# Performance work log

Hardware: AMD Instinct MI355X
Metric: run time of the kernel (lower is better)

Reference implementation:

```python
import jax, jax.numpy as jnp
import numpy as np

KERNEL = (7, 7)
NUM_CH = 4
EPS = 1e-06
ROPE_BASE = 10000.0


def _rel_dist():
    coords = [np.arange(k, dtype=np.float32) - k // 2 for k in KERNEL]
    g = np.meshgrid(*coords, indexing='ij')
    d = np.sqrt(sum(gi ** 2 for gi in g))
    return jnp.asarray(d.reshape(-1)), float(d.max())


def silu(x):
    return x * jax.nn.sigmoid(x)


def rmsnorm(x, w):
    rms = jnp.sqrt(jnp.mean(x * x, axis=-1, keepdims=True) + EPS)
    return x / rms * w


def apply_rope(x):
    # x: (B, L, H, D); positions run over dim -2 (matches torch default)
    H, D = x.shape[-2], x.shape[-1]
    half = D // 2
    pos = jnp.arange(H, dtype=jnp.float32)
    freqs = 1.0 / (ROPE_BASE ** (jnp.arange(half, dtype=x.dtype) / half))
    ang = pos[:, None] * freqs  # (H, half)
    cos, sin = jnp.cos(ang), jnp.sin(ang)
    x1, x2 = x[..., :half], x[..., half:2 * half]
    return jnp.concatenate([x1 * cos - x2 * sin, x1 * sin + x2 * cos], axis=-1)


def unfold2d(x):
    # x: (B, Hs, Ws, C) -> (B, Hs, Ws, k1*k2, C), row-major kernel order
    B, Hs, Ws, C = x.shape
    k1, k2 = KERNEL
    xp = jnp.pad(x, ((0, 0), ((k1 - 1) // 2, k1 // 2), ((k2 - 1) // 2, k2 // 2), (0, 0)))
    wins = [xp[:, i:i + Hs, j:j + Ws, :] for i in range(k1) for j in range(k2)]
    return jnp.stack(wins, axis=3)


def setup_inputs() -> dict:
    key = jax.random.key(0)
    ks = jax.random.split(key, 8)
    C = 256
    x = jax.random.normal(ks[0], (2, 64, 64, C), dtype=jnp.float32)
    W_qkv = jax.random.normal(ks[1], (C, 3 * C), dtype=jnp.float32) * 0.02
    w_qnorm = jnp.ones((C // NUM_CH,), dtype=jnp.float32)
    w_knorm = jnp.ones((C // NUM_CH,), dtype=jnp.float32)
    W_wp = jax.random.normal(ks[2], (C, 2 * NUM_CH), dtype=jnp.float32) * 0.02
    b_wp = jax.random.normal(ks[3], (2 * NUM_CH,), dtype=jnp.float32) * 0.02
    w_onorm = jnp.ones((C,), dtype=jnp.float32)
    W_out = jax.random.normal(ks[4], (C, C), dtype=jnp.float32) * 0.02
    W_gate = jax.random.normal(ks[5], (C, C), dtype=jnp.float32) * 0.02
    b_gate = 2.0 * jnp.ones((C,), dtype=jnp.float32)
    return {"x": x, "W_qkv": W_qkv, "w_qnorm": w_qnorm, "w_knorm": w_knorm,
            "W_wp": W_wp, "b_wp": b_wp, "w_onorm": w_onorm, "W_out": W_out,
            "W_gate": W_gate, "b_gate": b_gate}


def reference(x, W_qkv, w_qnorm, w_knorm, W_wp, b_wp, w_onorm, W_out, W_gate, b_gate):
    rel_dist, max_dist = _rel_dist()
    B, Hs, Ws, C = x.shape
    L = Hs * Ws
    H = NUM_CH
    D = C // H
    Wsz = KERNEL[0] * KERNEL[1]
    scale = D ** (-0.5)

    qkv = silu(x @ W_qkv)
    q, k, v = jnp.split(qkv, 3, axis=-1)

    q_flat = apply_rope(rmsnorm(q.reshape(B, L, H, D), w_qnorm))
    k_flat = apply_rope(rmsnorm(k.reshape(B, L, H, D), w_knorm))
    k = k_flat.reshape(B, Hs, Ws, C)

    wp = silu(x @ W_wp + b_wp)  # (B, Hs, Ws, 2H)
    width_raw, sharp_raw = jnp.split(wp, 2, axis=-1)
    width = jax.nn.sigmoid(width_raw) * max_dist + 0.5
    sharpness = jax.nn.sigmoid(sharp_raw) * 9.5 + 0.5

    k_win = unfold2d(k).reshape(B, L, Wsz, H, D)
    v_win = unfold2d(v).reshape(B, L, Wsz, H, D)

    scores = jnp.einsum('blhd,blwhd->blhw', q_flat, k_win) * scale
    width_f = width.reshape(B, L, H, 1)
    sharp_f = sharpness.reshape(B, L, H, 1)
    soft_mask = jax.nn.sigmoid((width_f - rel_dist) * sharp_f)
    scores = scores - (1.0 - soft_mask) * 10000.0
    attn = jax.nn.softmax(scores, axis=-1)

    out = jnp.einsum('blhw,blwhd->blhd', attn, v_win).reshape(B, Hs, Ws, C)
    out = rmsnorm(out, w_onorm)

    gate = jax.nn.sigmoid(silu(v @ W_gate + b_gate))
    merged = gate * v + (1.0 - gate) * out
    return silu(merged @ W_out)
```

## Files before the change

### kernel.cpp

```cpp
#include <hip/hip_runtime.h>
#include <hip/hip_fp16.h>
#include <math.h>

__device__ __forceinline__ float sigm(float x)  { return 1.0f / (1.0f + __expf(-x)); }
__device__ __forceinline__ float siluf(float x) { return x * sigm(x); }

typedef _Float16 half8  __attribute__((ext_vector_type(8)));
typedef _Float16 half4  __attribute__((ext_vector_type(4)));
typedef float    f32x4  __attribute__((ext_vector_type(4)));

__device__ __forceinline__ void gld16(const void* g, void* l) {
    __builtin_amdgcn_global_load_lds(
        (const __attribute__((address_space(1))) unsigned*)g,
        (__attribute__((address_space(3))) unsigned*)l, 16, 0, 0);
}

template <int MI, int AMODE>
__device__ __forceinline__ void gemm_core16(
    const __half* __restrict__ A16,
    const __half* __restrict__ Bhi, const __half* __restrict__ Blo,
    int nbs, int m0, int n0, int t, f32x4 (&acc)[MI][4])
{
    __shared__ short As[MI * 1024], BsHi[4096], BsLo[4096];
    const int lane = t & 63, wave = t >> 6;
    const int wm = (wave >> 1) * (MI << 4), wn = (wave & 1) << 6;
    const int fr = lane & 15, fq = lane >> 4;

    for (int kb = 0; kb < 8; ++kb) {
        __syncthreads();
#pragma unroll
        for (int hf = 0; hf < MI / 2; ++hf) {
            const int rr = wave * (MI << 3) + (hf << 4);
            size_t ga;
            if (AMODE == 0)
                ga = (((size_t)(kb * 8192 + m0 + rr)) << 5) + (lane << 3);
            else
                ga = (((size_t)(m0 + rr + (lane >> 2))) << 8) + (kb << 5) + ((lane & 3) << 3);
            gld16(A16 + ga, &As[rr << 5]);
        }
#pragma unroll
        for (int hf = 0; hf < 2; ++hf) {
            const int rr = (wave << 5) + (hf << 4);
            const size_t gb = (((size_t)(kb * nbs + n0 + rr)) << 5) + (lane << 3);
            gld16(Bhi + gb, &BsHi[rr << 5]);
            gld16(Blo + gb, &BsLo[rr << 5]);
        }
        __syncthreads();

        half8 a[MI], bh[4], bl[4];
#pragma unroll
        for (int i = 0; i < MI; ++i)
            a[i] = *(const half8*)&As[((wm + (i << 4) + fr) << 5) + (fq << 3)];
#pragma unroll
        for (int i = 0; i < 4; ++i) {
            const int boff = ((wn + (i << 4) + fr) << 5) + (fq << 3);
            bh[i] = *(const half8*)&BsHi[boff];
            bl[i] = *(const half8*)&BsLo[boff];
        }
#pragma unroll
        for (int mi = 0; mi < MI; ++mi)
#pragma unroll
            for (int ni = 0; ni < 4; ++ni) {
                acc[mi][ni] = __builtin_amdgcn_mfma_f32_16x16x32_f16(a[mi], bh[ni], acc[mi][ni], 0, 0, 0);
                acc[mi][ni] = __builtin_amdgcn_mfma_f32_16x16x32_f16(a[mi], bl[ni], acc[mi][ni], 0, 0, 0);
            }
    }
}

__global__ __launch_bounds__(256) void prep_kernel(
    const float* __restrict__ x, const float* __restrict__ Wqkv,
    const float* __restrict__ Wgate, const float* __restrict__ Wout,
    const float* __restrict__ Wwp, const float* __restrict__ bwp,
    __half* __restrict__ xh,
    __half* __restrict__ wqh, __half* __restrict__ wql,
    __half* __restrict__ wgh, __half* __restrict__ wgl,
    __half* __restrict__ woh, __half* __restrict__ wol,
    float* __restrict__ width, float* __restrict__ sharp)
{
    __shared__ float xs[32][260];
    const int t = threadIdx.x;
    const int blk = blockIdx.x;
    if (blk < 256) {
        const int row0 = blk << 5;
        for (int e = t; e < 2048; e += 256) {
            int r = e >> 6, cc = (e & 63) << 2;
            *(float4*)&xs[r][cc] = *(const float4*)&x[(size_t)(row0 + r) * 256 + cc];
        }
        __syncthreads();
        const int r = t >> 3, kb = t & 7;
        __half hibuf[32];
#pragma unroll
        for (int i = 0; i < 32; ++i)
            hibuf[i] = __float2half(xs[r][(kb << 5) + i]);
        const size_t ob = ((size_t)(kb * 8192 + row0 + r)) << 5;
#pragma unroll
        for (int i = 0; i < 4; ++i)
            *(int4*)&xh[ob + (i << 3)] = *(int4*)&hibuf[i << 3];
        float acc = 0.f;
#pragma unroll 8
        for (int k = 0; k < 256; ++k) acc += xs[r][k] * Wwp[k * 8 + kb];
        float s = sigm(siluf(acc + bwp[kb]));
        const int row = row0 + r;
        if (kb < 4) width[row * 4 + kb] = s * 4.242640687119285f + 0.5f;
        else        sharp[row * 4 + kb - 4] = s * 9.5f + 0.5f;
    } else {
        const float* W; __half *Whi, *Wlo; int N, nb0, ncnt;
        if (blk < 288)      { W = Wqkv;  Whi = wqh; Wlo = wql; N = 768; nb0 = (blk - 256) * 24; ncnt = 24; }
        else if (blk < 296) { W = Wgate; Whi = wgh; Wlo = wgl; N = 256; nb0 = (blk - 288) * 32; ncnt = 32; }
        else                { W = Wout;  Whi = woh; Wlo = wol; N = 256; nb0 = (blk - 296) * 32; ncnt = 32; }
        for (int j = 0; j < ncnt; ++j)
            xs[j][t] = W[(size_t)t * N + nb0 + j];
        __syncthreads();
        for (int c = t; c < ncnt * 8; c += 256) {
            const int j = c >> 3, kb = c & 7;
            __half hibuf[32], lobuf[32];
#pragma unroll
            for (int i = 0; i < 32; ++i) {
                float v = xs[j][(kb << 5) + i];
                __half hv = __float2half(v);
                hibuf[i] = hv;
                lobuf[i] = __float2half(v - __half2float(hv));
            }
            const size_t ob = ((size_t)(kb * N + nb0 + j)) << 5;
#pragma unroll
            for (int i = 0; i < 4; ++i) {
                *(int4*)&Whi[ob + (i << 3)] = *(int4*)&hibuf[i << 3];
                *(int4*)&Wlo[ob + (i << 3)] = *(int4*)&lobuf[i << 3];
            }
        }
    }
}

__global__ __launch_bounds__(256, 3) void gemm_qkv(
    const __half* __restrict__ xh,
    const __half* __restrict__ wqh, const __half* __restrict__ wql,
    const float* __restrict__ wq, const float* __restrict__ wk,
    __half* __restrict__ qh, __half* __restrict__ kh, __half* __restrict__ vh)
{
    const int t  = threadIdx.x;
    const int m0 = blockIdx.y << 7, n0 = blockIdx.x << 7;
    f32x4 acc[4][4] = {};
    gemm_core16<4, 0>(xh, wqh, wql, 768, m0, n0, t, acc);

    const int lane = t & 63, wave = t >> 6;
    const int wm = (wave >> 1) << 6, wn = (wave & 1) << 6;
    const int fr = lane & 15, fq = lane >> 4;
    const int gc0 = n0 + wn;
    const int seg = gc0 >> 8;
    const int h   = (gc0 >> 6) & 3;
    const int hc0 = h << 6;

#pragma unroll
    for (int mi = 0; mi < 4; ++mi)
#pragma unroll
        for (int ni = 0; ni < 4; ++ni)
#pragma unroll
            for (int r = 0; r < 4; ++r)
                acc[mi][ni][r] = siluf(acc[mi][ni][r]);

    if (seg == 2) {
#pragma unroll
        for (int mi = 0; mi < 4; ++mi)
#pragma unroll
            for (int r = 0; r < 4; ++r) {
                const size_t row = m0 + wm + (mi << 4) + (fq << 2) + r;
#pragma unroll
                for (int ni = 0; ni < 4; ++ni)
                    vh[row * 256 + hc0 + (ni << 4) + fr] = __float2half(acc[mi][ni][r]);
            }
    } else {
        const float* wnorm = seg ? wk : wq;
        float wv[4];
#pragma unroll
        for (int ni = 0; ni < 4; ++ni) wv[ni] = wnorm[(ni << 4) + fr];
        float cs[2], sn[2];
#pragma unroll
        for (int j = 0; j < 2; ++j) {
            const int d = (j << 4) + fr;
            const float freq = powf(10000.f, -(float)d * (1.f / 32.f));
            const float ang = (float)h * freq;
            cs[j] = cosf(ang); sn[j] = sinf(ang);
        }
        __half* dstbase = (seg ? kh : qh);
#pragma unroll
        for (int mi = 0; mi < 4; ++mi)
#pragma unroll
            for (int r = 0; r < 4; ++r) {
                float ss = acc[mi][0][r] * acc[mi][0][r] + acc[mi][1][r] * acc[mi][1][r]
                         + acc[mi][2][r] * acc[mi][2][r] + acc[mi][3][r] * acc[mi][3][r];
                ss += __shfl_xor(ss, 1); ss += __shfl_xor(ss, 2);
                ss += __shfl_xor(ss, 4); ss += __shfl_xor(ss, 8);
                const float rinv = 1.f / sqrtf(ss * (1.f / 64.f) + 1e-6f);
                float xv[4];
#pragma unroll
                for (int ni = 0; ni < 4; ++ni) xv[ni] = acc[mi][ni][r] * rinv * wv[ni];
                const float o0 = xv[0] * cs[0] - xv[2] * sn[0];
                const float o2 = xv[0] * sn[0] + xv[2] * cs[0];
                const float o1 = xv[1] * cs[1] - xv[3] * sn[1];
                const float o3 = xv[1] * sn[1] + xv[3] * cs[1];
                const size_t row = m0 + wm + (mi << 4) + (fq << 2) + r;
                __half* dst = dstbase + row * 256 + hc0;
                dst[fr]      = __float2half(o0);
                dst[16 + fr] = __float2half(o1);
                dst[32 + fr] = __float2half(o2);
                dst[48 + fr] = __float2half(o3);
            }
    }
}

__global__ __launch_bounds__(256, 3) void gemm_gate(
    const __half* __restrict__ vh,
    const __half* __restrict__ wgh, const __half* __restrict__ wgl,
    const float* __restrict__ bias, const float* __restrict__ attn_o,
    const float* __restrict__ sumsq4, const float* __restrict__ w_onorm,
    __half* __restrict__ mh)
{
    const int t  = threadIdx.x;
    const int m0 = blockIdx.y << 6, n0 = blockIdx.x << 7;
    f32x4 acc[2][4] = {};
    gemm_core16<2, 1>(vh, wgh, wgl, 256, m0, n0, t, acc);

    const int lane = t & 63, wave = t >> 6;
    const int wm = (wave >> 1) << 5, wn = (wave & 1) << 6;
    const int fr = lane & 15, fq = lane >> 4;

    float rmsf[2][4];
#pragma unroll
    for (int mi = 0; mi < 2; ++mi)
#pragma unroll
        for (int r = 0; r < 4; ++r) {
            const int m = m0 + wm + (mi << 4) + (fq << 2) + r;
            float4 s4 = *(const float4*)&sumsq4[(size_t)m * 4];
            rmsf[mi][r] = 1.f / sqrtf((s4.x + s4.y + s4.z + s4.w) * (1.f / 256.f) + 1e-6f);
        }

#pragma unroll
    for (int mi = 0; mi < 2; ++mi)
#pragma unroll
        for (int ni = 0; ni < 4; ++ni) {
            const int n  = n0 + wn + (ni << 4) + fr;
            const int mb = m0 + wm + (mi << 4) + (fq << 2);
            const float bb  = bias[n];
            const float won = w_onorm[n];
#pragma unroll
            for (int r = 0; r < 4; ++r) {
                const int m = mb + r;
                const float g  = sigm(siluf(acc[mi][ni][r] + bb));
                const float vv = __half2float(vh[(size_t)m * 256 + n]);
                const float oo = attn_o[(size_t)m * 256 + n] * rmsf[mi][r] * won;
                mh[(size_t)m * 256 + n] = __float2half(g * vv + (1.f - g) * oo);
            }
        }
}

__global__ __launch_bounds__(256, 3) void gemm_out(
    const __half* __restrict__ mh,
    const __half* __restrict__ woh, const __half* __restrict__ wol,
    float* __restrict__ out)
{
    const int t  = threadIdx.x;
    const int m0 = blockIdx.y << 6, n0 = blockIdx.x << 7;
    f32x4 acc[2][4] = {};
    gemm_core16<2, 1>(mh, woh, wol, 256, m0, n0, t, acc);

    const int lane = t & 63, wave = t >> 6;
    const int wm = (wave >> 1) << 5, wn = (wave & 1) << 6;
    const int fr = lane & 15, fq = lane >> 4;
#pragma unroll
    for (int mi = 0; mi < 2; ++mi)
#pragma unroll
        for (int ni = 0; ni < 4; ++ni) {
            const int n  = n0 + wn + (ni << 4) + fr;
            const int mb = m0 + wm + (mi << 4) + (fq << 2);
#pragma unroll
            for (int r = 0; r < 4; ++r)
                out[(size_t)(mb + r) * 256 + n] = siluf(acc[mi][ni][r]);
        }
}

#define PT 208

__global__ __launch_bounds__(256, 3) void attn_mfma(
    const __half* __restrict__ qh, const __half* __restrict__ kh,
    const __half* __restrict__ vh, const float* __restrict__ width,
    const float* __restrict__ sharp, float* __restrict__ attn_o,
    float* __restrict__ sumsq4)
{
    __shared__ short smem[26624];
    short* Ksh = smem;
    short* Psh = smem;
    short* Vt  = smem + 13312;

    const int t = threadIdx.x;
    const int lane = t & 63, wave = t >> 6;
    const int fr = lane & 15, fq = lane >> 4;
    const int patch = blockIdx.x, h = blockIdx.y, b = blockIdx.z;
    const int pr0 = (patch >> 3) << 3, pc0 = (patch & 7) << 3;
    const size_t cbase = (((size_t)b << 20)) + ((size_t)h << 6);

    float wd[4], sh[4]; int lq[4];
#pragma unroll
    for (int r = 0; r < 4; ++r) {
        const int q = (wave << 4) + (fq << 2) + r;
        lq[r] = (pr0 + (q >> 3)) * 64 + pc0 + (q & 7);
        wd[r] = width[((b << 12) + lq[r]) * 4 + h];
        sh[r] = sharp[((b << 12) + lq[r]) * 4 + h];
    }

    {
        const int lr = lane >> 3;
        const int doff = (((lane & 7) ^ (lr & 7)) << 3);
#pragma unroll
        for (int ci = 0; ci < 7; ++ci) {
            const int c = wave + (ci << 2);
            if (c < 26) {
                const int pr = (c << 3) + lr;
                const int pi = pr / 14, pj = pr - pi * 14;
                const int grc = min(max(pr0 - 3 + pi, 0), 63);
                const int gcc = min(max(pc0 - 3 + pj, 0), 63);
                gld16(kh + cbase + (size_t)((grc << 6) + gcc) * 256 + doff,
                      &Ksh[c << 9]);
            }
        }
    }

    const int qrow = (wave << 4) + fr;
    const int lqr = (pr0 + (qrow >> 3)) * 64 + pc0 + (qrow & 7);
    const __half* qptr = qh + (((size_t)(b << 12) + lqr) << 8) + (h << 6) + (fq << 3);
    half8 a0 = *(const half8*)qptr;
    half8 a1 = *(const half8*)(qptr + 32);

    const int srow = t >> 5;
    const int d2 = (t & 31) << 1;
    unsigned v0[13], v1[13];
#pragma unroll
    for (int j = 0; j < 13; ++j) {
        const int p = (j << 4) + (srow << 1);
#pragma unroll
        for (int e = 0; e < 2; ++e) {
            const int pp = p + e;
            const int pi = pp / 14, pj = pp - pi * 14;
            const int gr = pr0 - 3 + pi, gc = pc0 - 3 + pj;
            const bool ok = (pp < 196) & ((unsigned)gr < 64u) & ((unsigned)gc < 64u);
            const int grc = min(max(gr, 0), 63), gcc = min(max(gc, 0), 63);
            const unsigned vv = *(const unsigned*)(vh + cbase + (size_t)((grc << 6) + gcc) * 256 + d2);
            (e ? v1 : v0)[j] = ok ? vv : 0u;
        }
    }
#pragma unroll
    for (int j = 0; j < 13; ++j) {
        const int p = (j << 4) + (srow << 1);
        const unsigned lo = (v0[j] & 0xffffu) | (v1[j] << 16);
        const unsigned hi = (v0[j] >> 16) | (v1[j] & 0xffff0000u);
        *(unsigned*)&Vt[d2 * PT + p]       = lo;
        *(unsigned*)&Vt[(d2 + 1) * PT + p] = hi;
    }
    __syncthreads();

    f32x4 sc[13];
#pragma unroll
    for (int tl = 0; tl < 13; ++tl) {
        const int kr = (tl << 4) + fr;
        half8 b0 = *(const half8*)&Ksh[(kr << 6) + (((0 + fq) ^ (kr & 7)) << 3)];
        half8 b1 = *(const half8*)&Ksh[(kr << 6) + (((4 + fq) ^ (kr & 7)) << 3)];
        f32x4 z = {0.f, 0.f, 0.f, 0.f};
        z = __builtin_amdgcn_mfma_f32_16x16x32_f16(a0, b0, z, 0, 0, 0);
        sc[tl] = __builtin_amdgcn_mfma_f32_16x16x32_f16(a1, b1, z, 0, 0, 0);
    }

    float mx[4] = {-3e38f, -3e38f, -3e38f, -3e38f};
#pragma unroll
    for (int tl = 0; tl < 13; ++tl) {
        const int p = (tl << 4) + fr;
        const int pi = p / 14, pj = p - pi * 14;
        const bool pvld = p < 196;
        const bool inb = pvld & ((unsigned)(pr0 - 3 + pi) < 64u) & ((unsigned)(pc0 - 3 + pj) < 64u);
#pragma unroll
        for (int r = 0; r < 4; ++r) {
            const int q = (wave << 4) + (fq << 2) + r;
            const int di = pi - 3 - ((q >> 3) & 7), dj = pj - 3 - (q & 7);
            const bool win = pvld & ((unsigned)(di + 3) <= 6u) & ((unsigned)(dj + 3) <= 6u);
            const float rel = sqrtf((float)(di * di + dj * dj));
            const float mk = sigm((wd[r] - rel) * sh[r]);
            const float s0 = inb ? sc[tl][r] * 0.125f : 0.f;
            float s = s0 - (1.f - mk) * 10000.f;
            s = win ? s : -3e38f;
            sc[tl][r] = s;
            mx[r] = fmaxf(mx[r], s);
        }
    }
#pragma unroll
    for (int r = 0; r < 4; ++r) {
        mx[r] = fmaxf(mx[r], __shfl_xor(mx[r], 1));
        mx[r] = fmaxf(mx[r], __shfl_xor(mx[r], 2));
        mx[r] = fmaxf(mx[r], __shfl_xor(mx[r], 4));
        mx[r] = fmaxf(mx[r], __shfl_xor(mx[r], 8));
    }
    float sm[4] = {0.f, 0.f, 0.f, 0.f};
#pragma unroll
    for (int tl = 0; tl < 13; ++tl)
#pragma unroll
        for (int r = 0; r < 4; ++r) {
            const float e = __expf(sc[tl][r] - mx[r]);
            sc[tl][r] = e; sm[r] += e;
        }
#pragma unroll
    for (int r = 0; r < 4; ++r) {
        sm[r] += __shfl_xor(sm[r], 1);
        sm[r] += __shfl_xor(sm[r], 2);
        sm[r] += __shfl_xor(sm[r], 4);
        sm[r] += __shfl_xor(sm[r], 8);
        sm[r] = 1.f / sm[r];
    }

    __syncthreads();
#pragma unroll
    for (int tl = 0; tl < 13; ++tl)
#pragma unroll
        for (int r = 0; r < 4; ++r) {
            __half pv = __float2half(sc[tl][r] * sm[r]);
            Psh[((wave << 4) + (fq << 2) + r) * PT + (tl << 4) + fr] = *(short*)&pv;
        }
    asm volatile("s_waitcnt lgkmcnt(0)" ::: "memory");

    f32x4 o[4] = {};
    const int pra = (wave << 4) + fr;
#pragma unroll
    for (int s = 0; s < 6; ++s) {
        half8 pa = *(const half8*)&Psh[pra * PT + (fq << 3) + (s << 5)];
#pragma unroll
        for (int dt = 0; dt < 4; ++dt) {
            half8 vbf = *(const half8*)&Vt[((dt << 4) + fr) * PT + (fq << 3) + (s << 5)];
            o[dt] = __builtin_amdgcn_mfma_f32_16x16x32_f16(pa, vbf, o[dt], 0, 0, 0);
        }
    }
    {
        half4 pa = *(const half4*)&Psh[pra * PT + 192 + (fq << 2)];
#pragma unroll
        for (int dt = 0; dt < 4; ++dt) {
            half4 vbf = *(const half4*)&Vt[((dt << 4) + fr) * PT + 192 + (fq << 2)];
            o[dt] = __builtin_amdgcn_mfma_f32_16x16x16f16(pa, vbf, o[dt], 0, 0, 0);
        }
    }

#pragma unroll
    for (int r = 0; r < 4; ++r) {
        float ss = o[0][r]*o[0][r] + o[1][r]*o[1][r] + o[2][r]*o[2][r] + o[3][r]*o[3][r];
        ss += __shfl_xor(ss, 1); ss += __shfl_xor(ss, 2);
        ss += __shfl_xor(ss, 4); ss += __shfl_xor(ss, 8);
        const size_t rowb = (((size_t)(b << 12) + lq[r]) << 8) + h * 64;
#pragma unroll
        for (int dt = 0; dt < 4; ++dt)
            attn_o[rowb + (dt << 4) + fr] = o[dt][r];
        if (fr == 0) sumsq4[(((b << 12) + lq[r]) << 2) + h] = ss;
    }
}

extern "C" void kernel_launch(void* const* d_in, const int* in_sizes, int n_in,
                              void* d_out, int out_size, void* d_ws, size_t ws_size,
                              hipStream_t stream)
{
    const float* x      = (const float*)d_in[0];
    const float* W_qkv  = (const float*)d_in[1];
    const float* w_qn   = (const float*)d_in[2];
    const float* w_kn   = (const float*)d_in[3];
    const float* W_wp   = (const float*)d_in[4];
    const float* b_wp   = (const float*)d_in[5];
    const float* w_on   = (const float*)d_in[6];
    const float* W_out  = (const float*)d_in[7];
    const float* W_gate = (const float*)d_in[8];
    const float* b_gate = (const float*)d_in[9];
    float* out = (float*)d_out;

    __half* ws16 = (__half*)d_ws;
    __half* xh  = ws16;
    __half* wqh = xh  + 2097152;
    __half* wql = wqh + 196608;
    __half* wgh = wql + 196608;
    __half* wgl = wgh + 65536;
    __half* woh = wgl + 65536;
    __half* wol = woh + 65536;
    __half* qhp = wol + 65536;
    __half* khp = qhp + 2097152;
    __half* vhp = khp + 2097152;
    __half* mh  = vhp + 2097152;
    float* attn_o = (float*)(mh + 2097152);
    float* widthp = attn_o + 2097152;
    float* sharpp = widthp + 32768;
    float* sumsq4 = sharpp + 32768;

    prep_kernel<<<304, 256, 0, stream>>>(x, W_qkv, W_gate, W_out, W_wp, b_wp,
                                         xh, wqh, wql, wgh, wgl, woh, wol,
                                         widthp, sharpp);
    gemm_qkv<<<dim3(6, 64), 256, 0, stream>>>(xh, wqh, wql, w_qn, w_kn,
                                              qhp, khp, vhp);
    attn_mfma<<<dim3(64, 4, 2), 256, 0, stream>>>(qhp, khp, vhp, widthp, sharpp,
                                                  attn_o, sumsq4);
    gemm_gate<<<dim3(2, 128), 256, 0, stream>>>(vhp, wgh, wgl, b_gate,
                                                attn_o, sumsq4, w_on, mh);
    gemm_out<<<dim3(2, 128), 256, 0, stream>>>(mh, woh, wol, out);
}
```

Baseline: 156.6 us.

## Load K directly into registers and split P staging to cut LDS use

The attention kernel no longer stages the K window in shared memory. Each lane now loads its K fragments straight from global memory into registers, in three batches interleaved with the QK MFMAs. The probability tile is written to LDS in two halves of seven and six column tiles, each followed by a partial PV product, so the P buffer shrinks. Together these cut LDS from about 52KB to 40KB and raise the occupancy hint from 3 to 4 blocks. In exchange there is more register pressure, possible spills under the tighter launch bound, uncoalesced repeated K reads from global memory, and an extra barrier.

```diff
diff --git a/kernel.cpp b/kernel.cpp
--- a/kernel.cpp
+++ b/kernel.cpp
@@ -278,25 +278,25 @@
         }
 }
 
-#define PT 208
-
-__global__ __launch_bounds__(256, 3) void attn_mfma(
+#define PTV 208
+#define PTP 112
+
+__global__ __launch_bounds__(256, 4) void attn_mfma(
     const __half* __restrict__ qh, const __half* __restrict__ kh,
     const __half* __restrict__ vh, const float* __restrict__ width,
     const float* __restrict__ sharp, float* __restrict__ attn_o,
     float* __restrict__ sumsq4)
 {
-    __shared__ short smem[26624];
-    short* Ksh = smem;
-    short* Psh = smem;
-    short* Vt  = smem + 13312;
+    __shared__ short smem[20480];
+    short* Vt  = smem;
+    short* Psh = smem + 13312;
 
     const int t = threadIdx.x;
     const int lane = t & 63, wave = t >> 6;
     const int fr = lane & 15, fq = lane >> 4;
     const int patch = blockIdx.x, h = blockIdx.y, b = blockIdx.z;
     const int pr0 = (patch >> 3) << 3, pc0 = (patch & 7) << 3;
-    const size_t cbase = (((size_t)b << 20)) + ((size_t)h << 6);
+    const size_t cb0 = ((size_t)b << 20) + ((size_t)h << 6);
 
     float wd[4], sh[4]; int lq[4];
 #pragma unroll
@@ -306,29 +306,6 @@
         wd[r] = width[((b << 12) + lq[r]) * 4 + h];
         sh[r] = sharp[((b << 12) + lq[r]) * 4 + h];
     }
-
-    {
-        const int lr = lane >> 3;
-        const int doff = (((lane & 7) ^ (lr & 7)) << 3);
-#pragma unroll
-        for (int ci = 0; ci < 7; ++ci) {
-            const int c = wave + (ci << 2);
-            if (c < 26) {
-                const int pr = (c << 3) + lr;
-                const int pi = pr / 14, pj = pr - pi * 14;
-                const int grc = min(max(pr0 - 3 + pi, 0), 63);
-                const int gcc = min(max(pc0 - 3 + pj, 0), 63);
-                gld16(kh + cbase + (size_t)((grc << 6) + gcc) * 256 + doff,
-                      &Ksh[c << 9]);
-            }
-        }
-    }
-
-    const int qrow = (wave << 4) + fr;
-    const int lqr = (pr0 + (qrow >> 3)) * 64 + pc0 + (qrow & 7);
-    const __half* qptr = qh + (((size_t)(b << 12) + lqr) << 8) + (h << 6) + (fq << 3);
-    half8 a0 = *(const half8*)qptr;
-    half8 a1 = *(const half8*)(qptr + 32);
 
     const int srow = t >> 5;
     const int d2 = (t & 31) << 1;
@@ -343,7 +320,7 @@
             const int gr = pr0 - 3 + pi, gc = pc0 - 3 + pj;
             const bool ok = (pp < 196) & ((unsigned)gr < 64u) & ((unsigned)gc < 64u);
             const int grc = min(max(gr, 0), 63), gcc = min(max(gc, 0), 63);
-            const unsigned vv = *(const unsigned*)(vh + cbase + (size_t)((grc << 6) + gcc) * 256 + d2);
+            const unsigned vv = *(const unsigned*)(vh + cb0 + (size_t)((grc << 6) + gcc) * 256 + d2);
             (e ? v1 : v0)[j] = ok ? vv : 0u;
         }
     }
@@ -352,21 +329,61 @@
         const int p = (j << 4) + (srow << 1);
         const unsigned lo = (v0[j] & 0xffffu) | (v1[j] << 16);
         const unsigned hi = (v0[j] >> 16) | (v1[j] & 0xffff0000u);
-        *(unsigned*)&Vt[d2 * PT + p]       = lo;
-        *(unsigned*)&Vt[(d2 + 1) * PT + p] = hi;
-    }
-    __syncthreads();
+        *(unsigned*)&Vt[d2 * PTV + p]       = lo;
+        *(unsigned*)&Vt[(d2 + 1) * PTV + p] = hi;
+    }
+
+    const int qrow = (wave << 4) + fr;
+    const int lqr = (pr0 + (qrow >> 3)) * 64 + pc0 + (qrow & 7);
+    const __half* qptr = qh + cb0 + (size_t)lqr * 256 + (fq << 3);
+    half8 a0 = *(const half8*)qptr;
+    half8 a1 = *(const half8*)(qptr + 32);
 
     f32x4 sc[13];
-#pragma unroll
-    for (int tl = 0; tl < 13; ++tl) {
-        const int kr = (tl << 4) + fr;
-        half8 b0 = *(const half8*)&Ksh[(kr << 6) + (((0 + fq) ^ (kr & 7)) << 3)];
-        half8 b1 = *(const half8*)&Ksh[(kr << 6) + (((4 + fq) ^ (kr & 7)) << 3)];
+#define KADDR(tl) ({                                                        \
+        const int p_ = ((tl) << 4) + fr;                                    \
+        const int pi_ = p_ / 14, pj_ = p_ - pi_ * 14;                       \
+        const int grc_ = min(max(pr0 - 3 + pi_, 0), 63);                    \
+        const int gcc_ = min(max(pc0 - 3 + pj_, 0), 63);                    \
+        kh + cb0 + (size_t)((grc_ << 6) + gcc_) * 256 + (fq << 3); })
+
+    half8 k0a[5], k0b[5];
+#pragma unroll
+    for (int i = 0; i < 5; ++i) {
+        const __half* kp = KADDR(i);
+        k0a[i] = *(const half8*)kp; k0b[i] = *(const half8*)(kp + 32);
+    }
+    half8 k1a[4], k1b[4];
+#pragma unroll
+    for (int i = 0; i < 4; ++i) {
+        const __half* kp = KADDR(5 + i);
+        k1a[i] = *(const half8*)kp; k1b[i] = *(const half8*)(kp + 32);
+    }
+#pragma unroll
+    for (int i = 0; i < 5; ++i) {
         f32x4 z = {0.f, 0.f, 0.f, 0.f};
-        z = __builtin_amdgcn_mfma_f32_16x16x32_f16(a0, b0, z, 0, 0, 0);
-        sc[tl] = __builtin_amdgcn_mfma_f32_16x16x32_f16(a1, b1, z, 0, 0, 0);
-    }
+        z = __builtin_amdgcn_mfma_f32_16x16x32_f16(a0, k0a[i], z, 0, 0, 0);
+        sc[i] = __builtin_amdgcn_mfma_f32_16x16x32_f16(a1, k0b[i], z, 0, 0, 0);
+    }
+    half8 k2a[4], k2b[4];
+#pragma unroll
+    for (int i = 0; i < 4; ++i) {
+        const __half* kp = KADDR(9 + i);
+        k2a[i] = *(const half8*)kp; k2b[i] = *(const half8*)(kp + 32);
+    }
+#pragma unroll
+    for (int i = 0; i < 4; ++i) {
+        f32x4 z = {0.f, 0.f, 0.f, 0.f};
+        z = __builtin_amdgcn_mfma_f32_16x16x32_f16(a0, k1a[i], z, 0, 0, 0);
+        sc[5 + i] = __builtin_amdgcn_mfma_f32_16x16x32_f16(a1, k1b[i], z, 0, 0, 0);
+    }
+#pragma unroll
+    for (int i = 0; i < 4; ++i) {
+        f32x4 z = {0.f, 0.f, 0.f, 0.f};
+        z = __builtin_amdgcn_mfma_f32_16x16x32_f16(a0, k2a[i], z, 0, 0, 0);
+        sc[9 + i] = __builtin_amdgcn_mfma_f32_16x16x32_f16(a1, k2b[i], z, 0, 0, 0);
+    }
+#undef KADDR
 
     float mx[4] = {-3e38f, -3e38f, -3e38f, -3e38f};
 #pragma unroll
@@ -413,33 +430,53 @@
         sm[r] = 1.f / sm[r];
     }
 
-    __syncthreads();
-#pragma unroll
-    for (int tl = 0; tl < 13; ++tl)
+#pragma unroll
+    for (int tl = 0; tl < 7; ++tl)
 #pragma unroll
         for (int r = 0; r < 4; ++r) {
             __half pv = __float2half(sc[tl][r] * sm[r]);
-            Psh[((wave << 4) + (fq << 2) + r) * PT + (tl << 4) + fr] = *(short*)&pv;
-        }
-    asm volatile("s_waitcnt lgkmcnt(0)" ::: "memory");
+            Psh[((wave << 4) + (fq << 2) + r) * PTP + (tl << 4) + fr] = *(short*)&pv;
+        }
+    __syncthreads();
 
     f32x4 o[4] = {};
     const int pra = (wave << 4) + fr;
 #pragma unroll
-    for (int s = 0; s < 6; ++s) {
-        half8 pa = *(const half8*)&Psh[pra * PT + (fq << 3) + (s << 5)];
+    for (int s = 0; s < 3; ++s) {
+        half8 pa = *(const half8*)&Psh[pra * PTP + (fq << 3) + (s << 5)];
 #pragma unroll
         for (int dt = 0; dt < 4; ++dt) {
-            half8 vbf = *(const half8*)&Vt[((dt << 4) + fr) * PT + (fq << 3) + (s << 5)];
+            half8 vbf = *(const half8*)&Vt[((dt << 4) + fr) * PTV + (fq << 3) + (s << 5)];
             o[dt] = __builtin_amdgcn_mfma_f32_16x16x32_f16(pa, vbf, o[dt], 0, 0, 0);
         }
     }
     {
-        half4 pa = *(const half4*)&Psh[pra * PT + 192 + (fq << 2)];
+        half4 pa = *(const half4*)&Psh[pra * PTP + 96 + (fq << 2)];
 #pragma unroll
         for (int dt = 0; dt < 4; ++dt) {
-            half4 vbf = *(const half4*)&Vt[((dt << 4) + fr) * PT + 192 + (fq << 2)];
+            half4 vbf = *(const half4*)&Vt[((dt << 4) + fr) * PTV + 96 + (fq << 2)];
             o[dt] = __builtin_amdgcn_mfma_f32_16x16x16f16(pa, vbf, o[dt], 0, 0, 0);
+        }
+    }
+
+    __syncthreads();
+
+#pragma unroll
+    for (int tl = 7; tl < 13; ++tl)
+#pragma unroll
+        for (int r = 0; r < 4; ++r) {
+            __half pv = __float2half(sc[tl][r] * sm[r]);
+            Psh[((wave << 4) + (fq << 2) + r) * PTP + ((tl - 7) << 4) + fr] = *(short*)&pv;
+        }
+    asm volatile("s_waitcnt lgkmcnt(0)" ::: "memory");
+
+#pragma unroll
+    for (int s = 0; s < 3; ++s) {
+        half8 pa = *(const half8*)&Psh[pra * PTP + (fq << 3) + (s << 5)];
+#pragma unroll
+        for (int dt = 0; dt < 4; ++dt) {
+            half8 vbf = *(const half8*)&Vt[((dt << 4) + fr) * PTV + 112 + (fq << 3) + (s << 5)];
+            o[dt] = __builtin_amdgcn_mfma_f32_16x16x32_f16(pa, vbf, o[dt], 0, 0, 0);
         }
     }
 
```

Result: slower. 164.5 us (+5.0%).
